# Optimization experiments

Measured on AMD Instinct MI355X. Metric: run time of the kernel, lower is better.

Reference implementation:

```python
import math
import jax, jax.numpy as jnp
import numpy as np

KEY_SIZE = 128
VALUE_SIZE = 128


def setup_inputs() -> dict:
    key = jax.random.key(0)
    # channels = value_size + 2*key_size = 384
    x = jax.random.normal(key, (8, VALUE_SIZE + 2 * KEY_SIZE, 32, 32), dtype=jnp.float32)
    return {"x": x}


def _tokens(t):
    # [B, C, H, W] -> [B*H*W, C]  (matches view/transpose/view in torch code)
    B, C = t.shape[0], t.shape[1]
    return t.reshape(B, C, -1).transpose(0, 2, 1).reshape(-1, C)


def reference(x) -> jnp.ndarray:
    B, C, H, W = x.shape
    value = _tokens(x[:, :VALUE_SIZE])                      # [N, V]
    key_t = _tokens(x[:, VALUE_SIZE:VALUE_SIZE + KEY_SIZE])  # [N, K]
    query = _tokens(x[:, VALUE_SIZE + KEY_SIZE:])            # [N, K]
    # Global N x N attention over all batch*spatial positions (faithful to source)
    weight = (query @ key_t.T) / math.sqrt(KEY_SIZE)         # [N, N]
    attention = jax.nn.softmax(weight, axis=1) @ value      # [N, V]
    out = attention.reshape(B, H * W, VALUE_SIZE).transpose(0, 2, 1)
    return out.reshape(B, VALUE_SIZE, H, W)
```

## Files before the change

### kernel.cpp

```cpp
#include <hip/hip_runtime.h>
#include <hip/hip_bf16.h>
#include <stdint.h>

#define N_TOK 8192
#define DDIM  128

typedef _Float16 half2v __attribute__((ext_vector_type(2)));
typedef _Float16 half4v __attribute__((ext_vector_type(4)));
typedef _Float16 half8v __attribute__((ext_vector_type(8)));
typedef __fp16  fp16x2 __attribute__((ext_vector_type(2)));
typedef float f32x4 __attribute__((ext_vector_type(4)));
typedef half4v half4_ma __attribute__((may_alias));
typedef half8v half8_ma __attribute__((may_alias));
typedef float4 float4_ma __attribute__((may_alias));

#define MFMA16 __builtin_amdgcn_mfma_f32_16x16x16f16
#define MFMA32 __builtin_amdgcn_mfma_f32_16x16x32_f16

#define QSCALE (0.08838834764831845f * 1.4426950408889634f)

__device__ __forceinline__ half2v pkrtz(float a, float b) {
  return __builtin_bit_cast(half2v, __builtin_amdgcn_cvt_pkrtz(a, b));
}

#if __has_builtin(__builtin_amdgcn_fdot2)
__device__ __forceinline__ float dot2acc(half2v a, float c) {
  const fp16x2 ones = {(__fp16)1.f, (__fp16)1.f};
  return __builtin_amdgcn_fdot2(__builtin_bit_cast(fp16x2, a), ones, c, false);
}
#else
__device__ __forceinline__ float dot2acc(half2v a, float c) {
  return c + (float)a.x + (float)a.y;
}
#endif

__device__ __forceinline__ void gload_lds16(const _Float16* g, _Float16* l) {
  __builtin_amdgcn_global_load_lds(
      (const __attribute__((address_space(1))) void*)g,
      (__attribute__((address_space(3))) void*)l, 16, 0, 0);
}

__global__ void prep_all(const float* __restrict__ x,
                         _Float16* __restrict__ Qf, _Float16* __restrict__ Kf,
                         _Float16* __restrict__ Vt) {
  __shared__ float t[32][33];
  const int blk = blockIdx.x, tid = threadIdx.x;
  if (blk < 2048) {
    const int pt = blk & 31, ct = (blk >> 5) & 3, z = blk >> 7;
    const int b = z >> 1, isQ = z & 1;
    const int c0 = (isQ ? 256 : 128) + ct * 32;
    const int p0 = pt * 32;
    const int tx = tid & 31, ty0 = tid >> 5;
    const float* src = x + ((size_t)b * 384 + c0) * 1024 + p0;
#pragma unroll
    for (int i = 0; i < 4; ++i)
      t[ty0 + i * 8][tx] = src[(ty0 + i * 8) * 1024 + tx];
    __syncthreads();
    _Float16* dst = isQ ? Qf : Kf;
    const float sc = isQ ? QSCALE : 1.f;
#pragma unroll
    for (int i = 0; i < 4; ++i) {
      const int ty = ty0 + i * 8;
      dst[((size_t)b * 1024 + p0 + ty) * DDIM + ct * 32 + tx] = (_Float16)(t[tx][ty] * sc);
    }
  } else {
    const int i4 = ((blk - 2048) * 256 + tid) * 4;
    const int v = i4 >> 13, n = i4 & 8191;
    const int b = n >> 10, p = n & 1023;
    const float4 s = *(const float4_ma*)(x + ((size_t)b * 384 + v) * 1024 + p);
    half4v h; h.x = (_Float16)s.x; h.y = (_Float16)s.y; h.z = (_Float16)s.z; h.w = (_Float16)s.w;
    *(half4_ma*)(Vt + (size_t)v * N_TOK + b * 1024 + p) = h;
  }
}

template<int KS>
__global__ __launch_bounds__(512, 2) void flash_attn(
    const _Float16* __restrict__ Qf, const _Float16* __restrict__ Kf,
    const _Float16* __restrict__ Vt, _Float16* __restrict__ Opart,
    float* __restrict__ Lsum) {
  __shared__ _Float16 lds[32768];

  const int tid = threadIdx.x;
  const int w = tid >> 6, lane = tid & 63;
  const int quad = lane >> 4, l16 = lane & 15;
  const int blk = blockIdx.x;
  const int ks = (KS == 16) ? (((blk & 7) << 1) | (blk >> 8))
                            : (blk & 7);
  const int qt = (blk >> 3) & 31;
  const int kp = N_TOK / KS;
  const int chunks = kp >> 6;
  const int k0 = ks * kp;
  const int q0 = qt * 256;

  half8v qf[2][4];
#pragma unroll
  for (int t2 = 0; t2 < 2; ++t2) {
    const _Float16* qp = Qf + (size_t)(q0 + w * 32 + t2 * 16 + l16) * DDIM + quad * 8;
#pragma unroll
    for (int kb = 0; kb < 4; ++kb) qf[t2][kb] = *(const half8_ma*)(qp + kb * 32);
  }

  f32x4 O[2][8];
#pragma unroll
  for (int t2 = 0; t2 < 2; ++t2)
#pragma unroll
    for (int vb = 0; vb < 8; ++vb) O[t2][vb] = (f32x4){0.f, 0.f, 0.f, 0.f};
  float ls[2] = {0.f, 0.f};

  const _Float16* srcK[2];
  const _Float16* srcV[2];
  int slot[2];
#pragma unroll
  for (int j = 0; j < 2; ++j) {
    const int chi = w * 2 + j;
    srcK[j] = Kf + (size_t)(k0 + lane) * DDIM + chi * 8;
    const int t = chi * 64 + lane;
    const int v = t >> 3, h = t & 7;
    const int hs = h ^ ((v >> 1) & 7);
    srcV[j] = Vt + (size_t)v * N_TOK + k0 + hs * 8;
    slot[j] = chi * 512;
  }

#pragma unroll
  for (int j = 0; j < 2; ++j) {
    gload_lds16(srcK[j], lds + slot[j]);
    gload_lds16(srcV[j], lds + 8192 + slot[j]);
  }

  for (int ch = 0; ch < chunks; ++ch) {
    __syncthreads();
    _Float16* buf = lds + (ch & 1) * 16384;
    if (ch + 1 < chunks) {
      _Float16* nbuf = lds + ((ch + 1) & 1) * 16384;
      const int adv = (ch + 1) * 64;
#pragma unroll
      for (int j = 0; j < 2; ++j) {
        gload_lds16(srcK[j] + (size_t)adv * DDIM, nbuf + slot[j]);
        gload_lds16(srcV[j] + adv, nbuf + 8192 + slot[j]);
      }
    }
    const _Float16* Ksh = buf;
    const _Float16* Vsh = buf + 8192;

    f32x4 S[2][4];
#pragma unroll
    for (int t2 = 0; t2 < 2; ++t2)
#pragma unroll
      for (int cb = 0; cb < 4; ++cb) S[t2][cb] = (f32x4){0.f, 0.f, 0.f, 0.f};
#pragma unroll
    for (int kb = 0; kb < 4; ++kb) {
#pragma unroll
      for (int cb = 0; cb < 4; ++cb) {
        half8v kf = *(const half8_ma*)(Ksh + (((kb * 4 + quad) * 64) + cb * 16 + l16) * 8);
        S[0][cb] = MFMA32(kf, qf[0][kb], S[0][cb], 0, 0, 0);
        S[1][cb] = MFMA32(kf, qf[1][kb], S[1][cb], 0, 0, 0);
      }
    }

    half4v P[2][4];
#pragma unroll
    for (int t2 = 0; t2 < 2; ++t2) {
#pragma unroll
      for (int cb = 0; cb < 4; ++cb) {
        const float p0 = __builtin_amdgcn_exp2f(S[t2][cb][0]);
        const float p1 = __builtin_amdgcn_exp2f(S[t2][cb][1]);
        const float p2 = __builtin_amdgcn_exp2f(S[t2][cb][2]);
        const float p3 = __builtin_amdgcn_exp2f(S[t2][cb][3]);
        half2v lo = pkrtz(p0, p1);
        half2v hi = pkrtz(p2, p3);
        ls[t2] = dot2acc(lo, dot2acc(hi, ls[t2]));
        P[t2][cb] = __builtin_shufflevector(lo, hi, 0, 1, 2, 3);
      }
    }

#pragma unroll
    for (int cb = 0; cb < 4; ++cb) {
#pragma unroll
      for (int vb = 0; vb < 8; ++vb) {
        const int v = vb * 16 + l16;
        half4v vf = *(const half4_ma*)(Vsh + v * 64 + (((cb * 4 + quad) ^ (l16 & 14)) * 4));
        O[0][vb] = MFMA16(vf, P[0][cb], O[0][vb], 0, 0, 0);
        O[1][vb] = MFMA16(vf, P[1][cb], O[1][vb], 0, 0, 0);
      }
    }
  }

#pragma unroll
  for (int t2 = 0; t2 < 2; ++t2) {
    ls[t2] += __shfl_xor(ls[t2], 16, 64);
    ls[t2] += __shfl_xor(ls[t2], 32, 64);
  }
#pragma unroll
  for (int t2 = 0; t2 < 2; ++t2) {
    const float rl = 1.f / ls[t2];
    const int q = q0 + w * 32 + t2 * 16 + l16;
#pragma unroll
    for (int vb = 0; vb < 8; ++vb) {
#pragma unroll
      for (int r = 0; r < 4; ++r) {
        const int v = vb * 16 + quad * 4 + r;
        Opart[((size_t)ks * DDIM + v) * N_TOK + q] = (_Float16)(O[t2][vb][r] * rl);
      }
    }
  }
  if (lane < 16) {
#pragma unroll
    for (int t2 = 0; t2 < 2; ++t2)
      Lsum[(size_t)ks * N_TOK + q0 + w * 32 + t2 * 16 + lane] = ls[t2];
  }
}

__global__ void combine_kernel(const _Float16* __restrict__ Opart,
                               const float* __restrict__ Lsum,
                               float* __restrict__ out, int KS) {
  const int o4 = (blockIdx.x * 256 + threadIdx.x) * 4;
  const int b = o4 >> 17, v = (o4 >> 10) & 127, p = o4 & 1023;
  const int q = (b << 10) | p;
  float4 num = make_float4(0.f, 0.f, 0.f, 0.f);
  float4 den = make_float4(0.f, 0.f, 0.f, 0.f);
  for (int s = 0; s < KS; ++s) {
    const float4 l = *(const float4_ma*)(Lsum + (size_t)s * N_TOK + q);
    const half4v ov = *(const half4_ma*)(Opart + ((size_t)s * DDIM + v) * N_TOK + q);
    num.x += l.x * (float)ov.x; num.y += l.y * (float)ov.y;
    num.z += l.z * (float)ov.z; num.w += l.w * (float)ov.w;
    den.x += l.x; den.y += l.y; den.z += l.z; den.w += l.w;
  }
  *(float4_ma*)(out + o4) =
      make_float4(num.x / den.x, num.y / den.y, num.z / den.z, num.w / den.w);
}

extern "C" void kernel_launch(void* const* d_in, const int* in_sizes, int n_in,
                              void* d_out, int out_size, void* d_ws, size_t ws_size,
                              hipStream_t stream) {
  const float* x = (const float*)d_in[0];
  float* out = (float*)d_out;
  char* ws = (char*)d_ws;

  const size_t need16 = (6u << 20) + 16 * (2u << 20) + (size_t)16 * N_TOK * 4;
  const int KS = (ws_size >= need16) ? 16 : 8;

  _Float16* Qf    = (_Float16*)(ws);
  _Float16* Kf    = (_Float16*)(ws + (2u << 20));
  _Float16* Vt    = (_Float16*)(ws + (4u << 20));
  _Float16* Opart = (_Float16*)(ws + (6u << 20));
  float*    Lsum  = (float*)(ws + (6u << 20) + (size_t)KS * (2u << 20));

  prep_all<<<dim3(3072), dim3(256), 0, stream>>>(x, Qf, Kf, Vt);
  if (KS == 16) {
    flash_attn<16><<<dim3(512), dim3(512), 0, stream>>>(Qf, Kf, Vt, Opart, Lsum);
  } else {
    flash_attn<8><<<dim3(256), dim3(512), 0, stream>>>(Qf, Kf, Vt, Opart, Lsum);
  }
  combine_kernel<<<dim3(1024), dim3(256), 0, stream>>>(Opart, Lsum, out, KS);
}
```

Baseline: 116.4 us.

## Fuse prep, attention and combine into one persistent kernel with grid barriers

Merges the three launches (transpose/convert prep, split-K flash attention, combine) into a single kernel with 256 blocks, separated by atomic-counter grid barriers. This removes the launch gaps between the stages. It also fixes the key-split count at 8 and lowers occupancy to one block per CU, which leaves more CUs idle than the previous 512-block split-16 path. The barriers rely on every block being resident at once, and a memset is added to reset the barrier counter.

```diff
diff --git a/kernel.cpp b/kernel.cpp
--- a/kernel.cpp
+++ b/kernel.cpp
@@ -40,193 +40,212 @@
       (__attribute__((address_space(3))) void*)l, 16, 0, 0);
 }
 
-__global__ void prep_all(const float* __restrict__ x,
-                         _Float16* __restrict__ Qf, _Float16* __restrict__ Kf,
-                         _Float16* __restrict__ Vt) {
-  __shared__ float t[32][33];
-  const int blk = blockIdx.x, tid = threadIdx.x;
-  if (blk < 2048) {
-    const int pt = blk & 31, ct = (blk >> 5) & 3, z = blk >> 7;
-    const int b = z >> 1, isQ = z & 1;
-    const int c0 = (isQ ? 256 : 128) + ct * 32;
-    const int p0 = pt * 32;
-    const int tx = tid & 31, ty0 = tid >> 5;
-    const float* src = x + ((size_t)b * 384 + c0) * 1024 + p0;
-#pragma unroll
-    for (int i = 0; i < 4; ++i)
-      t[ty0 + i * 8][tx] = src[(ty0 + i * 8) * 1024 + tx];
-    __syncthreads();
-    _Float16* dst = isQ ? Qf : Kf;
-    const float sc = isQ ? QSCALE : 1.f;
-#pragma unroll
-    for (int i = 0; i < 4; ++i) {
-      const int ty = ty0 + i * 8;
-      dst[((size_t)b * 1024 + p0 + ty) * DDIM + ct * 32 + tx] = (_Float16)(t[tx][ty] * sc);
-    }
-  } else {
-    const int i4 = ((blk - 2048) * 256 + tid) * 4;
-    const int v = i4 >> 13, n = i4 & 8191;
-    const int b = n >> 10, p = n & 1023;
-    const float4 s = *(const float4_ma*)(x + ((size_t)b * 384 + v) * 1024 + p);
-    half4v h; h.x = (_Float16)s.x; h.y = (_Float16)s.y; h.z = (_Float16)s.z; h.w = (_Float16)s.w;
-    *(half4_ma*)(Vt + (size_t)v * N_TOK + b * 1024 + p) = h;
-  }
+__device__ __forceinline__ void grid_barrier(uint32_t* bar, uint32_t expected) {
+  __syncthreads();
+  if (threadIdx.x == 0) {
+    __threadfence();
+    __hip_atomic_fetch_add(bar, 1u, __ATOMIC_RELEASE, __HIP_MEMORY_SCOPE_AGENT);
+    while (__hip_atomic_load(bar, __ATOMIC_ACQUIRE, __HIP_MEMORY_SCOPE_AGENT) < expected)
+      __builtin_amdgcn_s_sleep(2);
+    __threadfence();
+  }
+  __syncthreads();
 }
 
 template<int KS>
-__global__ __launch_bounds__(512, 2) void flash_attn(
-    const _Float16* __restrict__ Qf, const _Float16* __restrict__ Kf,
-    const _Float16* __restrict__ Vt, _Float16* __restrict__ Opart,
-    float* __restrict__ Lsum) {
-  __shared__ _Float16 lds[32768];
+__global__ __launch_bounds__(512, 1) void fused_attn(
+    const float* __restrict__ x, float* __restrict__ out,
+    _Float16* __restrict__ Qf, _Float16* __restrict__ Kf,
+    _Float16* __restrict__ Vt, _Float16* __restrict__ Opart,
+    float* __restrict__ Lsum, uint32_t* __restrict__ bar) {
+  alignas(16) __shared__ _Float16 lds[32768];
 
   const int tid = threadIdx.x;
-  const int w = tid >> 6, lane = tid & 63;
-  const int quad = lane >> 4, l16 = lane & 15;
   const int blk = blockIdx.x;
-  const int ks = (KS == 16) ? (((blk & 7) << 1) | (blk >> 8))
-                            : (blk & 7);
-  const int qt = (blk >> 3) & 31;
-  const int kp = N_TOK / KS;
-  const int chunks = kp >> 6;
-  const int k0 = ks * kp;
-  const int q0 = qt * 256;
-
-  half8v qf[2][4];
-#pragma unroll
-  for (int t2 = 0; t2 < 2; ++t2) {
-    const _Float16* qp = Qf + (size_t)(q0 + w * 32 + t2 * 16 + l16) * DDIM + quad * 8;
-#pragma unroll
-    for (int kb = 0; kb < 4; ++kb) qf[t2][kb] = *(const half8_ma*)(qp + kb * 32);
-  }
-
-  f32x4 O[2][8];
-#pragma unroll
-  for (int t2 = 0; t2 < 2; ++t2)
-#pragma unroll
-    for (int vb = 0; vb < 8; ++vb) O[t2][vb] = (f32x4){0.f, 0.f, 0.f, 0.f};
-  float ls[2] = {0.f, 0.f};
-
-  const _Float16* srcK[2];
-  const _Float16* srcV[2];
-  int slot[2];
-#pragma unroll
-  for (int j = 0; j < 2; ++j) {
-    const int chi = w * 2 + j;
-    srcK[j] = Kf + (size_t)(k0 + lane) * DDIM + chi * 8;
-    const int t = chi * 64 + lane;
-    const int v = t >> 3, h = t & 7;
-    const int hs = h ^ ((v >> 1) & 7);
-    srcV[j] = Vt + (size_t)v * N_TOK + k0 + hs * 8;
-    slot[j] = chi * 512;
-  }
-
-#pragma unroll
-  for (int j = 0; j < 2; ++j) {
-    gload_lds16(srcK[j], lds + slot[j]);
-    gload_lds16(srcV[j], lds + 8192 + slot[j]);
-  }
-
-  for (int ch = 0; ch < chunks; ++ch) {
-    __syncthreads();
-    _Float16* buf = lds + (ch & 1) * 16384;
-    if (ch + 1 < chunks) {
-      _Float16* nbuf = lds + ((ch + 1) & 1) * 16384;
-      const int adv = (ch + 1) * 64;
-#pragma unroll
-      for (int j = 0; j < 2; ++j) {
-        gload_lds16(srcK[j] + (size_t)adv * DDIM, nbuf + slot[j]);
-        gload_lds16(srcV[j] + adv, nbuf + 8192 + slot[j]);
-      }
-    }
-    const _Float16* Ksh = buf;
-    const _Float16* Vsh = buf + 8192;
-
-    f32x4 S[2][4];
+  const int nblk = gridDim.x;
+
+  {
+    float* tbuf = (float*)lds;
+    const int team = tid >> 8, ttid = tid & 255;
+    const int tx = ttid & 31, ty0 = ttid >> 5;
+    for (int tile = blk * 2 + team; tile < 2048; tile += nblk * 2) {
+      const int pt = tile & 31, ct = (tile >> 5) & 3, z = tile >> 7;
+      const int b = z >> 1, isQ = z & 1;
+      const int c0 = (isQ ? 256 : 128) + ct * 32;
+      const int p0 = pt * 32;
+      float* t = tbuf + team * 1056;
+      const float* src = x + ((size_t)b * 384 + c0) * 1024 + p0;
+#pragma unroll
+      for (int i = 0; i < 4; ++i)
+        t[(ty0 + i * 8) * 33 + tx] = src[(ty0 + i * 8) * 1024 + tx];
+      __syncthreads();
+      _Float16* dst = isQ ? Qf : Kf;
+      const float sc = isQ ? QSCALE : 1.f;
+#pragma unroll
+      for (int i = 0; i < 4; ++i) {
+        const int ty = ty0 + i * 8;
+        dst[((size_t)b * 1024 + p0 + ty) * DDIM + ct * 32 + tx] =
+            (_Float16)(t[tx * 33 + ty] * sc);
+      }
+      __syncthreads();
+    }
+    for (int i4 = (blk * 512 + tid) * 4; i4 < DDIM * N_TOK; i4 += nblk * 512 * 4) {
+      const int v = i4 >> 13, n = i4 & 8191;
+      const int b = n >> 10, p = n & 1023;
+      const float4 s = *(const float4_ma*)(x + ((size_t)b * 384 + v) * 1024 + p);
+      half4v h; h.x = (_Float16)s.x; h.y = (_Float16)s.y;
+      h.z = (_Float16)s.z; h.w = (_Float16)s.w;
+      *(half4_ma*)(Vt + (size_t)v * N_TOK + b * 1024 + p) = h;
+    }
+  }
+  grid_barrier(bar + 0, nblk);
+
+  {
+    const int w = tid >> 6, lane = tid & 63;
+    const int quad = lane >> 4, l16 = lane & 15;
+    const int ks = (KS == 16) ? (((blk & 7) << 1) | (blk >> 8)) : (blk & (KS - 1));
+    const int qt = (blk / KS == 0 ? (blk >> 3) : (blk >> 3)) & 31;
+    const int kp = N_TOK / KS;
+    const int chunks = kp >> 6;
+    const int k0 = ks * kp;
+    const int q0 = ((blk >> 3) & 31) * 256;
+    (void)qt;
+
+    half8v qf[2][4];
+#pragma unroll
+    for (int t2 = 0; t2 < 2; ++t2) {
+      const _Float16* qp = Qf + (size_t)(q0 + w * 32 + t2 * 16 + l16) * DDIM + quad * 8;
+#pragma unroll
+      for (int kb = 0; kb < 4; ++kb) qf[t2][kb] = *(const half8_ma*)(qp + kb * 32);
+    }
+
+    f32x4 O[2][8];
 #pragma unroll
     for (int t2 = 0; t2 < 2; ++t2)
 #pragma unroll
-      for (int cb = 0; cb < 4; ++cb) S[t2][cb] = (f32x4){0.f, 0.f, 0.f, 0.f};
-#pragma unroll
-    for (int kb = 0; kb < 4; ++kb) {
+      for (int vb = 0; vb < 8; ++vb) O[t2][vb] = (f32x4){0.f, 0.f, 0.f, 0.f};
+    float ls[2] = {0.f, 0.f};
+
+    const _Float16* srcK[2];
+    const _Float16* srcV[2];
+    int slot[2];
+#pragma unroll
+    for (int j = 0; j < 2; ++j) {
+      const int chi = w * 2 + j;
+      srcK[j] = Kf + (size_t)(k0 + lane) * DDIM + chi * 8;
+      const int t = chi * 64 + lane;
+      const int v = t >> 3, h = t & 7;
+      const int hs = h ^ ((v >> 1) & 7);
+      srcV[j] = Vt + (size_t)v * N_TOK + k0 + hs * 8;
+      slot[j] = chi * 512;
+    }
+
+#pragma unroll
+    for (int j = 0; j < 2; ++j) {
+      gload_lds16(srcK[j], lds + slot[j]);
+      gload_lds16(srcV[j], lds + 8192 + slot[j]);
+    }
+
+    for (int ch = 0; ch < chunks; ++ch) {
+      __syncthreads();
+      _Float16* buf = lds + (ch & 1) * 16384;
+      if (ch + 1 < chunks) {
+        _Float16* nbuf = lds + ((ch + 1) & 1) * 16384;
+        const int adv = (ch + 1) * 64;
+#pragma unroll
+        for (int j = 0; j < 2; ++j) {
+          gload_lds16(srcK[j] + (size_t)adv * DDIM, nbuf + slot[j]);
+          gload_lds16(srcV[j] + adv, nbuf + 8192 + slot[j]);
+        }
+      }
+      const _Float16* Ksh = buf;
+      const _Float16* Vsh = buf + 8192;
+
+      f32x4 S[2][4];
+#pragma unroll
+      for (int t2 = 0; t2 < 2; ++t2)
+#pragma unroll
+        for (int cb = 0; cb < 4; ++cb) S[t2][cb] = (f32x4){0.f, 0.f, 0.f, 0.f};
+#pragma unroll
+      for (int kb = 0; kb < 4; ++kb) {
+#pragma unroll
+        for (int cb = 0; cb < 4; ++cb) {
+          half8v kf = *(const half8_ma*)(Ksh + (((kb * 4 + quad) * 64) + cb * 16 + l16) * 8);
+          S[0][cb] = MFMA32(kf, qf[0][kb], S[0][cb], 0, 0, 0);
+          S[1][cb] = MFMA32(kf, qf[1][kb], S[1][cb], 0, 0, 0);
+        }
+      }
+
+      half4v P[2][4];
+#pragma unroll
+      for (int t2 = 0; t2 < 2; ++t2) {
+#pragma unroll
+        for (int cb = 0; cb < 4; ++cb) {
+          const float p0 = __builtin_amdgcn_exp2f(S[t2][cb][0]);
+          const float p1 = __builtin_amdgcn_exp2f(S[t2][cb][1]);
+          const float p2 = __builtin_amdgcn_exp2f(S[t2][cb][2]);
+          const float p3 = __builtin_amdgcn_exp2f(S[t2][cb][3]);
+          half2v lo = pkrtz(p0, p1);
+          half2v hi = pkrtz(p2, p3);
+          ls[t2] = dot2acc(lo, dot2acc(hi, ls[t2]));
+          P[t2][cb] = __builtin_shufflevector(lo, hi, 0, 1, 2, 3);
+        }
+      }
+
 #pragma unroll
       for (int cb = 0; cb < 4; ++cb) {
-        half8v kf = *(const half8_ma*)(Ksh + (((kb * 4 + quad) * 64) + cb * 16 + l16) * 8);
-        S[0][cb] = MFMA32(kf, qf[0][kb], S[0][cb], 0, 0, 0);
-        S[1][cb] = MFMA32(kf, qf[1][kb], S[1][cb], 0, 0, 0);
-      }
-    }
-
-    half4v P[2][4];
+#pragma unroll
+        for (int vb = 0; vb < 8; ++vb) {
+          const int v = vb * 16 + l16;
+          half4v vf = *(const half4_ma*)(Vsh + v * 64 + (((cb * 4 + quad) ^ (l16 & 14)) * 4));
+          O[0][vb] = MFMA16(vf, P[0][cb], O[0][vb], 0, 0, 0);
+          O[1][vb] = MFMA16(vf, P[1][cb], O[1][vb], 0, 0, 0);
+        }
+      }
+    }
+
 #pragma unroll
     for (int t2 = 0; t2 < 2; ++t2) {
-#pragma unroll
-      for (int cb = 0; cb < 4; ++cb) {
-        const float p0 = __builtin_amdgcn_exp2f(S[t2][cb][0]);
-        const float p1 = __builtin_amdgcn_exp2f(S[t2][cb][1]);
-        const float p2 = __builtin_amdgcn_exp2f(S[t2][cb][2]);
-        const float p3 = __builtin_amdgcn_exp2f(S[t2][cb][3]);
-        half2v lo = pkrtz(p0, p1);
-        half2v hi = pkrtz(p2, p3);
-        ls[t2] = dot2acc(lo, dot2acc(hi, ls[t2]));
-        P[t2][cb] = __builtin_shufflevector(lo, hi, 0, 1, 2, 3);
-      }
-    }
-
-#pragma unroll
-    for (int cb = 0; cb < 4; ++cb) {
+      ls[t2] += __shfl_xor(ls[t2], 16, 64);
+      ls[t2] += __shfl_xor(ls[t2], 32, 64);
+    }
+#pragma unroll
+    for (int t2 = 0; t2 < 2; ++t2) {
+      const float rl = 1.f / ls[t2];
+      const int q = q0 + w * 32 + t2 * 16 + l16;
 #pragma unroll
       for (int vb = 0; vb < 8; ++vb) {
-        const int v = vb * 16 + l16;
-        half4v vf = *(const half4_ma*)(Vsh + v * 64 + (((cb * 4 + quad) ^ (l16 & 14)) * 4));
-        O[0][vb] = MFMA16(vf, P[0][cb], O[0][vb], 0, 0, 0);
-        O[1][vb] = MFMA16(vf, P[1][cb], O[1][vb], 0, 0, 0);
-      }
-    }
-  }
-
-#pragma unroll
-  for (int t2 = 0; t2 < 2; ++t2) {
-    ls[t2] += __shfl_xor(ls[t2], 16, 64);
-    ls[t2] += __shfl_xor(ls[t2], 32, 64);
-  }
-#pragma unroll
-  for (int t2 = 0; t2 < 2; ++t2) {
-    const float rl = 1.f / ls[t2];
-    const int q = q0 + w * 32 + t2 * 16 + l16;
-#pragma unroll
-    for (int vb = 0; vb < 8; ++vb) {
-#pragma unroll
-      for (int r = 0; r < 4; ++r) {
-        const int v = vb * 16 + quad * 4 + r;
-        Opart[((size_t)ks * DDIM + v) * N_TOK + q] = (_Float16)(O[t2][vb][r] * rl);
-      }
-    }
-  }
-  if (lane < 16) {
-#pragma unroll
-    for (int t2 = 0; t2 < 2; ++t2)
-      Lsum[(size_t)ks * N_TOK + q0 + w * 32 + t2 * 16 + lane] = ls[t2];
-  }
-}
-
-__global__ void combine_kernel(const _Float16* __restrict__ Opart,
-                               const float* __restrict__ Lsum,
-                               float* __restrict__ out, int KS) {
-  const int o4 = (blockIdx.x * 256 + threadIdx.x) * 4;
-  const int b = o4 >> 17, v = (o4 >> 10) & 127, p = o4 & 1023;
-  const int q = (b << 10) | p;
-  float4 num = make_float4(0.f, 0.f, 0.f, 0.f);
-  float4 den = make_float4(0.f, 0.f, 0.f, 0.f);
-  for (int s = 0; s < KS; ++s) {
-    const float4 l = *(const float4_ma*)(Lsum + (size_t)s * N_TOK + q);
-    const half4v ov = *(const half4_ma*)(Opart + ((size_t)s * DDIM + v) * N_TOK + q);
-    num.x += l.x * (float)ov.x; num.y += l.y * (float)ov.y;
-    num.z += l.z * (float)ov.z; num.w += l.w * (float)ov.w;
-    den.x += l.x; den.y += l.y; den.z += l.z; den.w += l.w;
-  }
-  *(float4_ma*)(out + o4) =
-      make_float4(num.x / den.x, num.y / den.y, num.z / den.z, num.w / den.w);
+#pragma unroll
+        for (int r = 0; r < 4; ++r) {
+          const int v = vb * 16 + quad * 4 + r;
+          Opart[((size_t)ks * DDIM + v) * N_TOK + q] = (_Float16)(O[t2][vb][r] * rl);
+        }
+      }
+    }
+    if (lane < 16) {
+#pragma unroll
+      for (int t2 = 0; t2 < 2; ++t2)
+        Lsum[(size_t)ks * N_TOK + q0 + w * 32 + t2 * 16 + lane] = ls[t2];
+    }
+  }
+  grid_barrier(bar + 8, nblk);
+
+  for (int o4 = (blk * 512 + tid) * 4; o4 < N_TOK * DDIM; o4 += nblk * 512 * 4) {
+    const int b = o4 >> 17, v = (o4 >> 10) & 127, p = o4 & 1023;
+    const int q = (b << 10) | p;
+    float4 num = make_float4(0.f, 0.f, 0.f, 0.f);
+    float4 den = make_float4(0.f, 0.f, 0.f, 0.f);
+#pragma unroll
+    for (int s = 0; s < KS; ++s) {
+      const float4 l = *(const float4_ma*)(Lsum + (size_t)s * N_TOK + q);
+      const half4v ov = *(const half4_ma*)(Opart + ((size_t)s * DDIM + v) * N_TOK + q);
+      num.x += l.x * (float)ov.x; num.y += l.y * (float)ov.y;
+      num.z += l.z * (float)ov.z; num.w += l.w * (float)ov.w;
+      den.x += l.x; den.y += l.y; den.z += l.z; den.w += l.w;
+    }
+    *(float4_ma*)(out + o4) =
+        make_float4(num.x / den.x, num.y / den.y, num.z / den.z, num.w / den.w);
+  }
 }
 
 extern "C" void kernel_launch(void* const* d_in, const int* in_sizes, int n_in,
@@ -236,20 +255,15 @@
   float* out = (float*)d_out;
   char* ws = (char*)d_ws;
 
-  const size_t need16 = (6u << 20) + 16 * (2u << 20) + (size_t)16 * N_TOK * 4;
-  const int KS = (ws_size >= need16) ? 16 : 8;
-
+  const int KS = 8;
   _Float16* Qf    = (_Float16*)(ws);
   _Float16* Kf    = (_Float16*)(ws + (2u << 20));
   _Float16* Vt    = (_Float16*)(ws + (4u << 20));
   _Float16* Opart = (_Float16*)(ws + (6u << 20));
   float*    Lsum  = (float*)(ws + (6u << 20) + (size_t)KS * (2u << 20));
-
-  prep_all<<<dim3(3072), dim3(256), 0, stream>>>(x, Qf, Kf, Vt);
-  if (KS == 16) {
-    flash_attn<16><<<dim3(512), dim3(512), 0, stream>>>(Qf, Kf, Vt, Opart, Lsum);
-  } else {
-    flash_attn<8><<<dim3(256), dim3(512), 0, stream>>>(Qf, Kf, Vt, Opart, Lsum);
-  }
-  combine_kernel<<<dim3(1024), dim3(256), 0, stream>>>(Opart, Lsum, out, KS);
-}
+  uint32_t* bar   = (uint32_t*)(ws + (6u << 20) + (size_t)KS * (2u << 20) + (1u << 20));
+
+  hipMemsetAsync(bar, 0, 64, stream);
+  fused_attn<8><<<dim3(32 * KS), dim3(512), 0, stream>>>(
+      x, out, Qf, Kf, Vt, Opart, Lsum, bar);
+}
```

After: 172.4 us. 48.2% more time.
